# Kernel tuning notes

Hardware: AMD Instinct MI355X
Metric: run time of the kernel (lower is better)

## Reference

```python
import jax, jax.numpy as jnp
import numpy as np

EPS = 1e-5
NUM_HEADS = 16
HEAD_DIM = 64


def layernorm(x, g, b):
    mu = jnp.mean(x, axis=-1, keepdims=True)
    var = jnp.mean(jnp.square(x - mu), axis=-1, keepdims=True)
    return (x - mu) * jax.lax.rsqrt(var + EPS) * g + b


def setup_inputs() -> dict:
    key = jax.random.key(0)
    ks = jax.random.split(key, 10)
    B, S, Q, D = 4, 4096, 256, 1024
    x = jax.random.normal(ks[0], (B, S, D), dtype=jnp.float32)
    queries = jax.random.normal(ks[1], (B, Q, D), dtype=jnp.float32)
    attn_mask = jax.random.randint(ks[2], (B, NUM_HEADS, Q, S), 0, 2) == 1
    key_padding_mask = jax.random.randint(ks[3], (B, S), 0, 2) == 1
    scale = 1.0 / np.sqrt(2.0 * D)  # xavier-ish
    Wq = jax.random.normal(ks[4], (D, D), dtype=jnp.float32) * scale
    Wk = jax.random.normal(ks[5], (D, D), dtype=jnp.float32) * scale
    Wv = jax.random.normal(ks[6], (D, D), dtype=jnp.float32) * scale
    Wo = jax.random.normal(ks[7], (D, D), dtype=jnp.float32) * scale
    ln1_g = jnp.ones((D,), jnp.float32); ln1_b = jnp.zeros((D,), jnp.float32)
    ln2_g = jnp.ones((D,), jnp.float32); ln2_b = jnp.zeros((D,), jnp.float32)
    return {"x": x, "queries": queries, "attn_mask": attn_mask,
            "key_padding_mask": key_padding_mask, "Wq": Wq, "Wk": Wk,
            "Wv": Wv, "Wo": Wo, "ln1_g": ln1_g, "ln1_b": ln1_b,
            "ln2_g": ln2_g, "ln2_b": ln2_b}


def reference(x, queries, attn_mask, key_padding_mask, Wq, Wk, Wv, Wo,
              ln1_g, ln1_b, ln2_g, ln2_b):
    B, S, D = x.shape
    Q = queries.shape[1]
    H, hd = NUM_HEADS, HEAD_DIM

    xn = layernorm(x, ln1_g, ln1_b)
    q = (queries @ Wq.T).reshape(B, Q, H, hd)
    k = (xn @ Wk.T).reshape(B, S, H, hd)
    v = (xn @ Wv.T).reshape(B, S, H, hd)

    # scores: (B, H, Q, S)
    scores = jnp.einsum('bqhd,bshd->bhqs', q, k) / np.sqrt(hd)

    mask = attn_mask | key_padding_mask[:, None, None, :]
    neg_inf = jnp.float32(-jnp.inf)
    masked = jnp.where(mask, neg_inf, scores)
    all_masked = jnp.all(mask, axis=-1, keepdims=True)  # rows fully masked
    safe = jnp.where(all_masked, 0.0, masked)
    attn = jax.nn.softmax(safe, axis=-1)
    attn = jnp.where(all_masked, 0.0, attn)

    out = jnp.einsum('bhqs,bshd->bqhd', attn, v).reshape(B, Q, D)
    out = layernorm(out, ln2_g, ln2_b)
    return out @ Wo.T, attn.mean(axis=1)
```

## Files before the change

kernel.cpp:

```cpp
#include <hip/hip_runtime.h>
#include <math.h>

#define DEV __device__ __forceinline__

typedef float  f4v  __attribute__((ext_vector_type(4)));
typedef __bf16 b8v  __attribute__((ext_vector_type(8)));
typedef short  s8v  __attribute__((ext_vector_type(8)));

DEV short f2b(float f){ __bf16 h = (__bf16)f; return __builtin_bit_cast(short, h); }
DEV float b2f(short s){ __bf16 h = __builtin_bit_cast(__bf16, s); return (float)h; }

DEV void gload16(const void* g, void* l){
  __builtin_amdgcn_global_load_lds((const __attribute__((address_space(1))) void*)g,
                                   (__attribute__((address_space(3))) void*)l, 16, 0, 0);
}

DEV b8v ldsf(const short* p){ return __builtin_bit_cast(b8v, *(const s8v*)p); }

DEV f4v mfma16(b8v a, b8v b, f4v c){ return __builtin_amdgcn_mfma_f32_16x16x32_bf16(a, b, c, 0, 0, 0); }

__global__ void cvt5_kernel(const float* __restrict__ s0, const float* __restrict__ s1,
                            const float* __restrict__ s2, const float* __restrict__ s3,
                            const float* __restrict__ s4,
                            short* __restrict__ d0, short* __restrict__ d1,
                            short* __restrict__ d2, short* __restrict__ d3,
                            short* __restrict__ d4){
  int i = blockIdx.x*256 + threadIdx.x;
  int buf = i >> 18, j = i & 262143;
  const float* s = (buf==0)?s0:(buf==1)?s1:(buf==2)?s2:(buf==3)?s3:s4;
  short*       d = (buf==0)?d0:(buf==1)?d1:(buf==2)?d2:(buf==3)?d3:d4;
  float4 v = ((const float4*)s)[j];
  ((short4*)d)[j] = make_short4(f2b(v.x), f2b(v.y), f2b(v.z), f2b(v.w));
}

__global__ __launch_bounds__(256) void ln_kernel(const float* __restrict__ x, const float* __restrict__ gg,
                                                 const float* __restrict__ bb, short* __restrict__ out){
  int row = blockIdx.x, tid = threadIdx.x;
  const float4 v = ((const float4*)(x + (size_t)row*1024))[tid];
  float s = v.x + v.y + v.z + v.w;
  #pragma unroll
  for (int off=1; off<64; off<<=1) s += __shfl_xor(s, off);
  __shared__ float red[4];
  if ((tid&63)==0) red[tid>>6] = s;
  __syncthreads();
  float mu = (red[0]+red[1]+red[2]+red[3]) * (1.0f/1024.0f);
  float d0=v.x-mu, d1=v.y-mu, d2=v.z-mu, d3=v.w-mu;
  float q = d0*d0 + d1*d1 + d2*d2 + d3*d3;
  #pragma unroll
  for (int off=1; off<64; off<<=1) q += __shfl_xor(q, off);
  __syncthreads();
  if ((tid&63)==0) red[tid>>6] = q;
  __syncthreads();
  float rs = rsqrtf((red[0]+red[1]+red[2]+red[3]) * (1.0f/1024.0f) + 1e-5f);
  float4 g4 = ((const float4*)gg)[tid];
  float4 b4 = ((const float4*)bb)[tid];
  short4 o = make_short4(f2b(d0*rs*g4.x + b4.x), f2b(d1*rs*g4.y + b4.y),
                         f2b(d2*rs*g4.z + b4.z), f2b(d3*rs*g4.w + b4.w));
  ((short4*)(out + (size_t)row*1024))[tid] = o;
}

__global__ __launch_bounds__(256) void ln_reduce_kernel(const short* __restrict__ opart, const float* __restrict__ gg,
                                                        const float* __restrict__ bb, short* __restrict__ out){
  int row = blockIdx.x, tid = threadIdx.x;
  float a0=0.f, a1=0.f, a2=0.f, a3=0.f;
  #pragma unroll
  for (int sc=0; sc<16; ++sc){
    short4 t = ((const short4*)(opart + ((size_t)sc*1024 + row)*1024))[tid];
    a0 += b2f(t.x); a1 += b2f(t.y); a2 += b2f(t.z); a3 += b2f(t.w);
  }
  float s = a0 + a1 + a2 + a3;
  #pragma unroll
  for (int off=1; off<64; off<<=1) s += __shfl_xor(s, off);
  __shared__ float red[4];
  if ((tid&63)==0) red[tid>>6] = s;
  __syncthreads();
  float mu = (red[0]+red[1]+red[2]+red[3]) * (1.0f/1024.0f);
  float d0=a0-mu, d1=a1-mu, d2=a2-mu, d3=a3-mu;
  float q = d0*d0 + d1*d1 + d2*d2 + d3*d3;
  #pragma unroll
  for (int off=1; off<64; off<<=1) q += __shfl_xor(q, off);
  __syncthreads();
  if ((tid&63)==0) red[tid>>6] = q;
  __syncthreads();
  float rs = rsqrtf((red[0]+red[1]+red[2]+red[3]) * (1.0f/1024.0f) + 1e-5f);
  float4 g4 = ((const float4*)gg)[tid];
  float4 b4 = ((const float4*)bb)[tid];
  short4 o = make_short4(f2b(d0*rs*g4.x + b4.x), f2b(d1*rs*g4.y + b4.y),
                         f2b(d2*rs*g4.z + b4.z), f2b(d3*rs*g4.w + b4.w));
  ((short4*)(out + (size_t)row*1024))[tid] = o;
}

template<int OUTF32>
__global__ __launch_bounds__(256) void gemm_small(const short* __restrict__ A, const short* __restrict__ B,
                                                  void* __restrict__ C, int M, int N, int K){
  __shared__ short sA[2][64*64];
  __shared__ short sB[2][64*64];
  int tid=threadIdx.x, lane=tid&63, wv=tid>>6, g=lane>>4, r=lane&15;
  int wr=wv>>1, wc=wv&1;
  int m0=blockIdx.x*64, n0=blockIdx.y*64;
  f4v z = {0.f,0.f,0.f,0.f};
  f4v acc[2][2];
  #pragma unroll
  for (int i=0;i<2;++i){
    #pragma unroll
    for (int j=0;j<2;++j) acc[i][j]=z;
  }
  auto stage = [&](int buf, int kt){
    #pragma unroll
    for (int i=0;i<2;++i){
      int idx = i*256 + tid;
      int row = idx>>3, cbs = (idx&7)^(row&7);
      gload16(A + (size_t)(m0+row)*K + kt*64 + cbs*8, &sA[buf][(i*256+wv*64)*8]);
      gload16(B + (size_t)(n0+row)*K + kt*64 + cbs*8, &sB[buf][(i*256+wv*64)*8]);
    }
  };
  int nkt = K >> 6;
  stage(0, 0);
  __syncthreads();
  for (int kt=0; kt<nkt; ++kt){
    int cur = kt & 1;
    if (kt+1 < nkt) stage(cur^1, kt+1);
    b8v af[2][2], bf[2][2];
    #pragma unroll
    for (int mf=0;mf<2;++mf){
      #pragma unroll
      for (int ks=0;ks<2;++ks){
        int ra = wr*32 + mf*16 + r;
        int rb = wc*32 + mf*16 + r;
        af[mf][ks] = ldsf(&sA[cur][ra*64 + (((ks*4+g)^(ra&7))*8)]);
        bf[mf][ks] = ldsf(&sB[cur][rb*64 + (((ks*4+g)^(rb&7))*8)]);
      }
    }
    #pragma unroll
    for (int mf=0;mf<2;++mf){
      #pragma unroll
      for (int nf=0;nf<2;++nf){
        acc[mf][nf] = mfma16(af[mf][0], bf[nf][0], acc[mf][nf]);
        acc[mf][nf] = mfma16(af[mf][1], bf[nf][1], acc[mf][nf]);
      }
    }
    __syncthreads();
  }
  #pragma unroll
  for (int mf=0;mf<2;++mf){
    #pragma unroll
    for (int nf=0;nf<2;++nf){
      #pragma unroll
      for (int j=0;j<4;++j){
        int m = m0 + wr*32 + mf*16 + g*4 + j;
        int n = n0 + wc*32 + nf*16 + r;
        if (OUTF32) ((float*)C)[(size_t)m*N + n] = acc[mf][nf][j];
        else        ((short*)C)[(size_t)m*N + n] = f2b(acc[mf][nf][j]);
      }
    }
  }
}

__global__ __launch_bounds__(512,2) void gemm_dual_bt(const short* __restrict__ A, const short* __restrict__ B0,
                                                      const short* __restrict__ B1, short* __restrict__ C0,
                                                      short* __restrict__ C1, int M, int N, int K){
  __shared__ short sA[2][256*32];
  __shared__ short sB0[2][128*32];
  __shared__ short sB1[2][128*32];
  int tid=threadIdx.x, lane=tid&63, wv=tid>>6, g=lane>>4, r=lane&15;
  int wr=wv>>1, wc=wv&1;
  int m0=blockIdx.x*256, n0=blockIdx.y*128;
  f4v z = {0.f,0.f,0.f,0.f};
  f4v a0[4][4], a1[4][4];
  #pragma unroll
  for (int i=0;i<4;++i){
    #pragma unroll
    for (int j=0;j<4;++j){ a0[i][j]=z; a1[i][j]=z; }
  }
  auto stage = [&](int buf, int kt){
    #pragma unroll
    for (int i=0;i<2;++i){
      int idx = i*512 + tid;
      int row = idx>>2, sl = idx&3;
      gload16(A + (size_t)(m0+row)*K + kt*32 + sl*8, &sA[buf][(i*512+wv*64)*8]);
    }
    {
      int row = tid>>2, sl = tid&3;
      gload16(B0 + (size_t)(n0+row)*K + kt*32 + sl*8, &sB0[buf][(wv*64)*8]);
      gload16(B1 + (size_t)(n0+row)*K + kt*32 + sl*8, &sB1[buf][(wv*64)*8]);
    }
  };
  int nkt = K >> 5;
  stage(0, 0);
  __syncthreads();
  for (int kt=0; kt<nkt; ++kt){
    int cur = kt & 1;
    if (kt+1 < nkt) stage(cur^1, kt+1);
    b8v af[4], b0f[4], b1f[4];
    #pragma unroll
    for (int mf=0;mf<4;++mf) af[mf] = ldsf(&sA[cur][(wr*64+mf*16+r)*32 + g*8]);
    #pragma unroll
    for (int nf=0;nf<4;++nf){
      b0f[nf] = ldsf(&sB0[cur][(wc*64+nf*16+r)*32 + g*8]);
      b1f[nf] = ldsf(&sB1[cur][(wc*64+nf*16+r)*32 + g*8]);
    }
    #pragma unroll
    for (int mf=0;mf<4;++mf){
      #pragma unroll
      for (int nf=0;nf<4;++nf){
        a0[mf][nf] = mfma16(af[mf], b0f[nf], a0[mf][nf]);
        a1[mf][nf] = mfma16(af[mf], b1f[nf], a1[mf][nf]);
      }
    }
    __syncthreads();
  }
  #pragma unroll
  for (int mf=0;mf<4;++mf){
    #pragma unroll
    for (int nf=0;nf<4;++nf){
      #pragma unroll
      for (int j=0;j<4;++j){
        int m = m0 + wr*64 + mf*16 + g*4 + j;
        int n = n0 + wc*64 + nf*16 + r;
        C0[(size_t)m*N + n] = f2b(a0[mf][nf][j]);
        C1[(size_t)m*N + n] = f2b(a1[mf][nf][j]);
      }
    }
  }
}

__global__ __launch_bounds__(256) void vtrans_kernel(const short* __restrict__ v, short* __restrict__ vt){
  int bid = blockIdx.x;
  int sb = bid & 63, bh = bid >> 6;
  int b = bh >> 4, h = bh & 15;
  int s0 = sb*64;
  __shared__ short t[64][80];
  int tid = threadIdx.x;
  #pragma unroll
  for (int i=0;i<2;++i){
    int idx = tid + i*256;
    int row = idx>>3, sl = idx&7;
    *(s8v*)&t[row][sl*8] = *(const s8v*)(v + (size_t)(b*4096 + s0 + row)*1024 + h*64 + sl*8);
  }
  __syncthreads();
  int hd = tid>>2, part = tid&3;
  s8v o0, o1;
  #pragma unroll
  for (int j=0;j<8;++j){ o0[j] = t[part*16+j][hd]; o1[j] = t[part*16+8+j][hd]; }
  size_t base = (size_t)(bh*64+hd)*4096 + s0 + part*16;
  *(s8v*)(vt + base)     = o0;
  *(s8v*)(vt + base + 8) = o1;
}

__global__ __launch_bounds__(256,2) void lsum_kernel(const short* __restrict__ qp, const short* __restrict__ kb,
                                                     const int* __restrict__ am, const int* __restrict__ kpm,
                                                     unsigned* __restrict__ pm, float* __restrict__ lpart){
  int bid = blockIdx.x;
  int sc = bid & 15, bh = bid >> 4;
  int b = bh >> 4, h = bh & 15;
  int s0 = sc*256;
  __shared__ short sQ[256*64];
  __shared__ short sK[256*64];
  __shared__ unsigned sPM[256*8];
  __shared__ unsigned kw[8];
  int tid=threadIdx.x, lane=tid&63, wv=tid>>6, g=lane>>4, r=lane&15;

  #pragma unroll
  for (int i=0;i<8;++i){
    int idx = i*256 + wv*64 + lane;
    int row = idx>>3, cbs = (idx&7)^(row&7);
    gload16(qp + (size_t)(b*256 + row)*1024 + h*64 + cbs*8, &sQ[(i*256+wv*64)*8]);
  }
  #pragma unroll
  for (int i=0;i<8;++i){
    int idx = i*256 + wv*64 + lane;
    int row = idx>>3, cbs = (idx&7)^(row&7);
    gload16(kb + (size_t)(b*4096 + s0 + row)*1024 + h*64 + cbs*8, &sK[(i*256+wv*64)*8]);
  }
  if (tid < 8){
    unsigned bits = 0;
    const int4* kp = (const int4*)(kpm + (size_t)b*4096 + s0 + tid*32);
    #pragma unroll
    for (int j=0;j<8;++j){
      int4 t = kp[j];
      bits |= (unsigned)(t.x!=0) << (j*4+0);
      bits |= (unsigned)(t.y!=0) << (j*4+1);
      bits |= (unsigned)(t.z!=0) << (j*4+2);
      bits |= (unsigned)(t.w!=0) << (j*4+3);
    }
    kw[tid] = bits;
  }
  unsigned rowbits[8];
  const int4* ap = (const int4*)(am + (size_t)(bh*256 + tid)*4096 + s0);
  #pragma unroll
  for (int w=0;w<8;++w){
    unsigned bits = 0;
    #pragma unroll
    for (int j=0;j<8;++j){
      int4 t = ap[w*8+j];
      bits |= (unsigned)(t.x!=0) << (j*4+0);
      bits |= (unsigned)(t.y!=0) << (j*4+1);
      bits |= (unsigned)(t.z!=0) << (j*4+2);
      bits |= (unsigned)(t.w!=0) << (j*4+3);
    }
    rowbits[w] = bits;
  }
  __syncthreads();
  #pragma unroll
  for (int w=0;w<8;++w){
    unsigned mword = rowbits[w] | kw[w];
    sPM[tid*8+w] = mword;
    pm[(size_t)bid*2048 + tid*8 + w] = mword;
  }
  __syncthreads();

  b8v a[4][2];
  #pragma unroll
  for (int mf=0;mf<4;++mf){
    #pragma unroll
    for (int ks=0;ks<2;++ks){
      int q = wv*64 + mf*16 + r;
      a[mf][ks] = ldsf(&sQ[q*64 + (((ks*4+g)^(q&7))*8)]);
    }
  }
  float lacc[4][4];
  #pragma unroll
  for (int mf=0;mf<4;++mf){
    #pragma unroll
    for (int j=0;j<4;++j) lacc[mf][j] = 0.f;
  }
  f4v z = {0.f,0.f,0.f,0.f};
  #pragma unroll 4
  for (int nf=0;nf<16;++nf){
    int srow = nf*16 + r;
    b8v b0 = ldsf(&sK[srow*64 + ((g^(srow&7))*8)]);
    b8v b1 = ldsf(&sK[srow*64 + (((4+g)^(srow&7))*8)]);
    f4v acc[4];
    #pragma unroll
    for (int mf=0;mf<4;++mf){
      acc[mf] = mfma16(a[mf][0], b0, z);
      acc[mf] = mfma16(a[mf][1], b1, acc[mf]);
    }
    #pragma unroll
    for (int mf=0;mf<4;++mf){
      #pragma unroll
      for (int j=0;j<4;++j){
        int q = wv*64 + mf*16 + g*4 + j;
        unsigned wm = sPM[q*8 + (nf>>1)];
        bool mskd = (wm >> ((nf&1)*16 + r)) & 1u;
        lacc[mf][j] += mskd ? 0.f : __expf(acc[mf][j]*0.125f);
      }
    }
  }
  #pragma unroll
  for (int off=1; off<16; off<<=1){
    #pragma unroll
    for (int mf=0;mf<4;++mf){
      #pragma unroll
      for (int j=0;j<4;++j) lacc[mf][j] += __shfl_xor(lacc[mf][j], off);
    }
  }
  if (r == 0){
    #pragma unroll
    for (int mf=0;mf<4;++mf){
      #pragma unroll
      for (int j=0;j<4;++j){
        int q = wv*64 + mf*16 + g*4 + j;
        lpart[(size_t)bid*256 + q] = lacc[mf][j];
      }
    }
  }
}

__global__ void lcomb_kernel(const float* __restrict__ lpart, float* __restrict__ linv){
  int row = blockIdx.x*256 + threadIdx.x;
  int q = row & 255, bh = row >> 8;
  float l = 0.f;
  #pragma unroll
  for (int sc=0; sc<16; ++sc) l += lpart[(size_t)(bh*16+sc)*256 + q];
  linv[row] = (l > 0.f) ? (1.0f/l) : 0.f;
}

__global__ __launch_bounds__(512,2) void attn_pv_kernel(const short* __restrict__ qp, const short* __restrict__ kb,
                                                        const short* __restrict__ vt, const unsigned* __restrict__ pm,
                                                        const float* __restrict__ linv, short* __restrict__ opart,
                                                        float* __restrict__ out2){
  int bid = blockIdx.x;
  int sc = bid & 15, qt = (bid>>4)&3, b = bid>>6;
  int s0 = sc*256, q0 = qt*64;
  __shared__ short sK[256*64];
  __shared__ short sV[64*256];
  __shared__ short sQ[64*64];
  __shared__ unsigned sPM[64*8];
  int tid=threadIdx.x, lane=tid&63, wv=tid>>6, g=lane>>4, r=lane&15;
  int wq = wv>>2, ws = wv&3;
  f4v z = {0.f,0.f,0.f,0.f};
  float macc[2][4][4];
  #pragma unroll
  for (int mf=0;mf<2;++mf){
    #pragma unroll
    for (int nf=0;nf<4;++nf){
      #pragma unroll
      for (int j=0;j<4;++j) macc[mf][nf][j] = 0.f;
    }
  }

  for (int h=0; h<16; ++h){
    int bh = b*16 + h;
    __syncthreads();
    {
      int row = tid>>3, cbs = (tid&7)^(row&7);
      gload16(qp + (size_t)(b*256 + q0 + row)*1024 + h*64 + cbs*8, &sQ[(wv*64)*8]);
    }
    #pragma unroll
    for (int i=0;i<4;++i){
      int idx = i*512 + tid;
      int row = idx>>3, cbs = (idx&7)^(row&7);
      gload16(kb + (size_t)(b*4096 + s0 + row)*1024 + h*64 + cbs*8, &sK[(i*512+wv*64)*8]);
    }
    #pragma unroll
    for (int i=0;i<4;++i){
      int idx = i*512 + tid;
      int row = idx>>5, sl = idx&31, sls = sl^(row&7);
      gload16(vt + (size_t)(bh*64 + row)*4096 + s0 + sls*8, &sV[(i*512+wv*64)*8]);
    }
    {
      int row = tid>>3, w = tid&7;
      sPM[tid] = pm[(size_t)(bh*16+sc)*2048 + (q0+row)*8 + w];
    }
    __syncthreads();

    b8v aq[2][2];
    #pragma unroll
    for (int mf=0;mf<2;++mf){
      #pragma unroll
      for (int ks=0;ks<2;++ks){
        int qrow = wq*32 + mf*16 + r;
        aq[mf][ks] = ldsf(&sQ[qrow*64 + (((ks*4+g)^(qrow&7))*8)]);
      }
    }
    f4v accs[2][4];
    #pragma unroll
    for (int mf=0;mf<2;++mf){
      #pragma unroll
      for (int nf=0;nf<4;++nf) accs[mf][nf] = z;
    }
    #pragma unroll
    for (int nf=0;nf<4;++nf){
      int srow = ws*64 + nf*16 + r;
      b8v b0 = ldsf(&sK[srow*64 + ((g^(srow&7))*8)]);
      b8v b1 = ldsf(&sK[srow*64 + (((4+g)^(srow&7))*8)]);
      #pragma unroll
      for (int mf=0;mf<2;++mf){
        accs[mf][nf] = mfma16(aq[mf][0], b0, accs[mf][nf]);
        accs[mf][nf] = mfma16(aq[mf][1], b1, accs[mf][nf]);
      }
    }
    __syncthreads();

    #pragma unroll
    for (int mf=0;mf<2;++mf){
      #pragma unroll
      for (int j=0;j<4;++j){
        int ql = wq*32 + mf*16 + g*4 + j;
        float iv = linv[(size_t)bh*256 + q0 + ql];
        #pragma unroll
        for (int nf=0;nf<4;++nf){
          unsigned wm = sPM[ql*8 + ws*2 + (nf>>1)];
          bool mskd = (wm >> ((nf&1)*16 + r)) & 1u;
          float p = mskd ? 0.f : __expf(accs[mf][nf][j]*0.125f) * iv;
          macc[mf][nf][j] += p;
          int sl_ = ws*64 + nf*16 + r;
          sK[ql*256 + (((sl_>>3)^(ql&7))*8) + (sl_&7)] = f2b(p);
        }
      }
    }
    __syncthreads();

    f4v acco[2]; acco[0]=z; acco[1]=z;
    #pragma unroll
    for (int ks=0;ks<8;++ks){
      int vrow = ws*16 + r;
      b8v bv = ldsf(&sV[vrow*256 + (((ks*4+g)^(vrow&7))*8)]);
      #pragma unroll
      for (int mf=0;mf<2;++mf){
        int prow = wq*32 + mf*16 + r;
        b8v ap = ldsf(&sK[prow*256 + (((ks*4+g)^(prow&7))*8)]);
        acco[mf] = mfma16(ap, bv, acco[mf]);
      }
    }
    #pragma unroll
    for (int mf=0;mf<2;++mf){
      #pragma unroll
      for (int j=0;j<4;++j)
        opart[((size_t)sc*1024 + b*256 + q0 + wq*32 + mf*16 + g*4 + j)*1024 + h*64 + ws*16 + r] = f2b(acco[mf][j]);
    }
  }

  #pragma unroll
  for (int mf=0;mf<2;++mf){
    #pragma unroll
    for (int nf=0;nf<4;++nf){
      #pragma unroll
      for (int j=0;j<4;++j){
        int q = q0 + wq*32 + mf*16 + g*4 + j;
        int s = s0 + ws*64 + nf*16 + r;
        out2[(size_t)(b*256 + q)*4096 + s] = macc[mf][nf][j] * 0.0625f;
      }
    }
  }
}

extern "C" void kernel_launch(void* const* d_in, const int* in_sizes, int n_in,
                              void* d_out, int out_size, void* d_ws, size_t ws_size,
                              hipStream_t stream){
  const float* x       = (const float*)d_in[0];
  const float* queries = (const float*)d_in[1];
  const int*   am      = (const int*)d_in[2];
  const int*   kpm     = (const int*)d_in[3];
  const float* Wq      = (const float*)d_in[4];
  const float* Wk      = (const float*)d_in[5];
  const float* Wv      = (const float*)d_in[6];
  const float* Wo      = (const float*)d_in[7];
  const float* ln1g    = (const float*)d_in[8];
  const float* ln1b    = (const float*)d_in[9];
  const float* ln2g    = (const float*)d_in[10];
  const float* ln2b    = (const float*)d_in[11];
  float* out0 = (float*)d_out;
  float* out2 = out0 + (size_t)4*256*1024;
  char* ws = (char*)d_ws;

  size_t off = 0;
  auto alloc = [&](size_t bytes){ void* p = ws + off; off += (bytes + 255) & ~(size_t)255; return p; };
  short*    xn   = (short*)alloc(33554432);
  short*    vt   = xn;
  short*    kb   = (short*)alloc(33554432);
  short*    vb   = (short*)alloc(33554432);
  short*    wqb  = (short*)alloc(2097152);
  short*    wkb  = (short*)alloc(2097152);
  short*    wvb  = (short*)alloc(2097152);
  short*    wob  = (short*)alloc(2097152);
  short*    qbf  = (short*)alloc(2097152);
  short*    qpj  = (short*)alloc(2097152);
  unsigned* pmw  = (unsigned*)alloc(8388608);
  float*    lpart= (float*)alloc(1048576);
  float*    linv = (float*)alloc(65536);
  short*    opart= (short*)alloc(33554432);
  short*    onb  = (short*)alloc(2097152);

  cvt5_kernel<<<5120,256,0,stream>>>(queries, Wq, Wk, Wv, Wo, qbf, wqb, wkb, wvb, wob);
  ln_kernel<<<16384,256,0,stream>>>(x, ln1g, ln1b, xn);
  gemm_dual_bt<<<dim3(64,8),512,0,stream>>>(xn, wkb, wvb, kb, vb, 16384, 1024, 1024);
  gemm_small<0><<<dim3(16,16),256,0,stream>>>(qbf, wqb, qpj, 1024, 1024, 1024);
  vtrans_kernel<<<4096,256,0,stream>>>(vb, vt);
  lsum_kernel<<<1024,256,0,stream>>>(qpj, kb, am, kpm, pmw, lpart);
  lcomb_kernel<<<64,256,0,stream>>>(lpart, linv);
  attn_pv_kernel<<<256,512,0,stream>>>(qpj, kb, vt, pmw, linv, opart, out2);
  ln_reduce_kernel<<<1024,256,0,stream>>>(opart, ln2g, ln2b, onb);
  gemm_small<1><<<dim3(16,16),256,0,stream>>>(onb, wob, out0, 1024, 1024, 1024);
}
```

Measured before the change: 340.1 us.

## Double-buffer attn_pv head loop and build mask bits with coalesced ballots

In attn_pv, the Q, K, V and mask tiles for the next head are prefetched into a second LDS buffer while the current head computes. The QK MFMA is transposed so probabilities are packed and stored to LDS and out2 as vectors, and LDS-only barriers are used between phases. In lsum, the per-thread strided conversion of the mask rows is replaced by lane-coalesced loads combined with __ballot, and mask words are cached in registers for the exp loop. The trade-off is that doubling the LDS buffers (about 148KB) likely allows only one attn_pv block per CU instead of the two requested by the launch bounds.

```diff
diff --git a/kernel.cpp b/kernel.cpp
--- a/kernel.cpp
+++ b/kernel.cpp
@@ -18,6 +18,11 @@
 DEV b8v ldsf(const short* p){ return __builtin_bit_cast(b8v, *(const s8v*)p); }
 
 DEV f4v mfma16(b8v a, b8v b, f4v c){ return __builtin_amdgcn_mfma_f32_16x16x32_bf16(a, b, c, 0, 0, 0); }
+
+DEV void lds_barrier(){
+  asm volatile("s_waitcnt lgkmcnt(0)" ::: "memory");
+  __builtin_amdgcn_s_barrier();
+}
 
 __global__ void cvt5_kernel(const float* __restrict__ s0, const float* __restrict__ s1,
                             const float* __restrict__ s2, const float* __restrict__ s3,
@@ -257,7 +262,6 @@
   __shared__ short sQ[256*64];
   __shared__ short sK[256*64];
   __shared__ unsigned sPM[256*8];
-  __shared__ unsigned kw[8];
   int tid=threadIdx.x, lane=tid&63, wv=tid>>6, g=lane>>4, r=lane&15;
 
   #pragma unroll
@@ -272,40 +276,23 @@
     int row = idx>>3, cbs = (idx&7)^(row&7);
     gload16(kb + (size_t)(b*4096 + s0 + row)*1024 + h*64 + cbs*8, &sK[(i*256+wv*64)*8]);
   }
-  if (tid < 8){
-    unsigned bits = 0;
-    const int4* kp = (const int4*)(kpm + (size_t)b*4096 + s0 + tid*32);
-    #pragma unroll
-    for (int j=0;j<8;++j){
-      int4 t = kp[j];
-      bits |= (unsigned)(t.x!=0) << (j*4+0);
-      bits |= (unsigned)(t.y!=0) << (j*4+1);
-      bits |= (unsigned)(t.z!=0) << (j*4+2);
-      bits |= (unsigned)(t.w!=0) << (j*4+3);
-    }
-    kw[tid] = bits;
-  }
-  unsigned rowbits[8];
-  const int4* ap = (const int4*)(am + (size_t)(bh*256 + tid)*4096 + s0);
-  #pragma unroll
-  for (int w=0;w<8;++w){
-    unsigned bits = 0;
-    #pragma unroll
-    for (int j=0;j<8;++j){
-      int4 t = ap[w*8+j];
-      bits |= (unsigned)(t.x!=0) << (j*4+0);
-      bits |= (unsigned)(t.y!=0) << (j*4+1);
-      bits |= (unsigned)(t.z!=0) << (j*4+2);
-      bits |= (unsigned)(t.w!=0) << (j*4+3);
-    }
-    rowbits[w] = bits;
-  }
-  __syncthreads();
-  #pragma unroll
-  for (int w=0;w<8;++w){
-    unsigned mword = rowbits[w] | kw[w];
-    sPM[tid*8+w] = mword;
-    pm[(size_t)bid*2048 + tid*8 + w] = mword;
+  int4 kp = *(const int4*)(kpm + (size_t)b*4096 + s0 + lane*4);
+  bool k0 = kp.x!=0, k1 = kp.y!=0, k2 = kp.z!=0, k3 = kp.w!=0;
+  #pragma unroll 4
+  for (int i=0;i<64;++i){
+    int row = wv*64 + i;
+    const int4 t = *(const int4*)(am + (size_t)(bh*256 + row)*4096 + s0 + lane*4);
+    unsigned long long m0 = __ballot(k0 || (t.x!=0));
+    unsigned long long m1 = __ballot(k1 || (t.y!=0));
+    unsigned long long m2 = __ballot(k2 || (t.z!=0));
+    unsigned long long m3 = __ballot(k3 || (t.w!=0));
+    if (lane < 8){
+      int jj = lane>>1, hh = lane&1;
+      unsigned long long bj = (jj==0)?m0:((jj==1)?m1:((jj==2)?m2:m3));
+      unsigned w = (unsigned)(bj >> (hh*32));
+      sPM[row*8 + lane] = w;
+      pm[(size_t)bid*2048 + row*8 + lane] = w;
+    }
   }
   __syncthreads();
 
@@ -316,6 +303,16 @@
     for (int ks=0;ks<2;++ks){
       int q = wv*64 + mf*16 + r;
       a[mf][ks] = ldsf(&sQ[q*64 + (((ks*4+g)^(q&7))*8)]);
+    }
+  }
+  unsigned wmr[4][4][2];
+  #pragma unroll
+  for (int mf=0;mf<4;++mf){
+    #pragma unroll
+    for (int jq=0;jq<4;++jq){
+      int q = wv*64 + mf*16 + g*4 + jq;
+      wmr[mf][jq][0] = sPM[q*8 + (r&3)*2 + 0];
+      wmr[mf][jq][1] = sPM[q*8 + (r&3)*2 + 1];
     }
   }
   float lacc[4][4];
@@ -336,13 +333,12 @@
       acc[mf] = mfma16(a[mf][0], b0, z);
       acc[mf] = mfma16(a[mf][1], b1, acc[mf]);
     }
+    int bitp = 4*(nf&7) + (r>>2);
     #pragma unroll
     for (int mf=0;mf<4;++mf){
       #pragma unroll
       for (int j=0;j<4;++j){
-        int q = wv*64 + mf*16 + g*4 + j;
-        unsigned wm = sPM[q*8 + (nf>>1)];
-        bool mskd = (wm >> ((nf&1)*16 + r)) & 1u;
+        bool mskd = (wmr[mf][j][nf>>3] >> bitp) & 1u;
         lacc[mf][j] += mskd ? 0.f : __expf(acc[mf][j]*0.125f);
       }
     }
@@ -383,104 +379,122 @@
   int bid = blockIdx.x;
   int sc = bid & 15, qt = (bid>>4)&3, b = bid>>6;
   int s0 = sc*256, q0 = qt*64;
-  __shared__ short sK[256*64];
-  __shared__ short sV[64*256];
-  __shared__ short sQ[64*64];
-  __shared__ unsigned sPM[64*8];
+  __shared__ short sK[2][256*64];
+  __shared__ short sV[2][64*256];
+  __shared__ short sQ[2][64*64];
+  __shared__ unsigned sPM[2][64*8];
   int tid=threadIdx.x, lane=tid&63, wv=tid>>6, g=lane>>4, r=lane&15;
   int wq = wv>>2, ws = wv&3;
   f4v z = {0.f,0.f,0.f,0.f};
-  float macc[2][4][4];
-  #pragma unroll
-  for (int mf=0;mf<2;++mf){
-    #pragma unroll
-    for (int nf=0;nf<4;++nf){
-      #pragma unroll
-      for (int j=0;j<4;++j) macc[mf][nf][j] = 0.f;
-    }
-  }
-
-  for (int h=0; h<16; ++h){
+  float macc[4][2][4];
+  #pragma unroll
+  for (int sb=0;sb<4;++sb){
+    #pragma unroll
+    for (int qb=0;qb<2;++qb){
+      #pragma unroll
+      for (int j=0;j<4;++j) macc[sb][qb][j] = 0.f;
+    }
+  }
+
+  auto stage = [&](int buf, int h){
     int bh = b*16 + h;
-    __syncthreads();
-    {
-      int row = tid>>3, cbs = (tid&7)^(row&7);
-      gload16(qp + (size_t)(b*256 + q0 + row)*1024 + h*64 + cbs*8, &sQ[(wv*64)*8]);
-    }
+    { int row = tid>>3, cbs = (tid&7)^(row&7);
+      gload16(qp + (size_t)(b*256 + q0 + row)*1024 + h*64 + cbs*8, &sQ[buf][(wv*64)*8]); }
     #pragma unroll
     for (int i=0;i<4;++i){
       int idx = i*512 + tid;
       int row = idx>>3, cbs = (idx&7)^(row&7);
-      gload16(kb + (size_t)(b*4096 + s0 + row)*1024 + h*64 + cbs*8, &sK[(i*512+wv*64)*8]);
+      gload16(kb + (size_t)(b*4096 + s0 + row)*1024 + h*64 + cbs*8, &sK[buf][(i*512+wv*64)*8]);
     }
     #pragma unroll
     for (int i=0;i<4;++i){
       int idx = i*512 + tid;
       int row = idx>>5, sl = idx&31, sls = sl^(row&7);
-      gload16(vt + (size_t)(bh*64 + row)*4096 + s0 + sls*8, &sV[(i*512+wv*64)*8]);
-    }
-    {
-      int row = tid>>3, w = tid&7;
-      sPM[tid] = pm[(size_t)(bh*16+sc)*2048 + (q0+row)*8 + w];
-    }
-    __syncthreads();
-
-    b8v aq[2][2];
-    #pragma unroll
-    for (int mf=0;mf<2;++mf){
+      gload16(vt + (size_t)(bh*64 + row)*4096 + s0 + sls*8, &sV[buf][(i*512+wv*64)*8]);
+    }
+  };
+  auto pmload = [&](int h)->unsigned {
+    return pm[(size_t)((b*16+h)*16+sc)*2048 + (q0 + (tid>>3))*8 + (tid&7)];
+  };
+
+  stage(0, 0);
+  sPM[0][tid] = pmload(0);
+  __syncthreads();
+
+  for (int h=0; h<16; ++h){
+    int cur = h&1;
+    unsigned pmnext = 0;
+    if (h < 15){
+      stage(cur^1, h+1);
+      pmnext = pmload(h+1);
+    }
+    int bh = b*16 + h;
+
+    b8v qf[2][2];
+    #pragma unroll
+    for (int qb=0;qb<2;++qb){
       #pragma unroll
       for (int ks=0;ks<2;++ks){
-        int qrow = wq*32 + mf*16 + r;
-        aq[mf][ks] = ldsf(&sQ[qrow*64 + (((ks*4+g)^(qrow&7))*8)]);
-      }
-    }
-    f4v accs[2][4];
-    #pragma unroll
-    for (int mf=0;mf<2;++mf){
-      #pragma unroll
-      for (int nf=0;nf<4;++nf) accs[mf][nf] = z;
-    }
-    #pragma unroll
-    for (int nf=0;nf<4;++nf){
-      int srow = ws*64 + nf*16 + r;
-      b8v b0 = ldsf(&sK[srow*64 + ((g^(srow&7))*8)]);
-      b8v b1 = ldsf(&sK[srow*64 + (((4+g)^(srow&7))*8)]);
-      #pragma unroll
-      for (int mf=0;mf<2;++mf){
-        accs[mf][nf] = mfma16(aq[mf][0], b0, accs[mf][nf]);
-        accs[mf][nf] = mfma16(aq[mf][1], b1, accs[mf][nf]);
-      }
-    }
-    __syncthreads();
-
-    #pragma unroll
-    for (int mf=0;mf<2;++mf){
-      #pragma unroll
-      for (int j=0;j<4;++j){
-        int ql = wq*32 + mf*16 + g*4 + j;
-        float iv = linv[(size_t)bh*256 + q0 + ql];
+        int qrow = wq*32 + qb*16 + r;
+        qf[qb][ks] = ldsf(&sQ[cur][qrow*64 + (((ks*4+g)^(qrow&7))*8)]);
+      }
+    }
+    f4v accs[4][2];
+    #pragma unroll
+    for (int sb=0;sb<4;++sb){
+      int srow = ws*64 + sb*16 + r;
+      b8v k0 = ldsf(&sK[cur][srow*64 + ((g^(srow&7))*8)]);
+      b8v k1 = ldsf(&sK[cur][srow*64 + (((4+g)^(srow&7))*8)]);
+      #pragma unroll
+      for (int qb=0;qb<2;++qb){
+        accs[sb][qb] = mfma16(k0, qf[qb][0], z);
+        accs[sb][qb] = mfma16(k1, qf[qb][1], accs[sb][qb]);
+      }
+    }
+    lds_barrier();
+
+    float iv[2];
+    iv[0] = linv[(size_t)bh*256 + q0 + wq*32 + r];
+    iv[1] = linv[(size_t)bh*256 + q0 + wq*32 + 16 + r];
+    unsigned wmq[2][4];
+    #pragma unroll
+    for (int qb=0;qb<2;++qb){
+      #pragma unroll
+      for (int j=0;j<4;++j)
+        wmq[qb][j] = sPM[cur][(wq*32+qb*16+r)*8 + j*2 + (ws>>1)];
+    }
+    short* P = &sK[cur][0];
+    #pragma unroll
+    for (int sb=0;sb<4;++sb){
+      int bitp = (ws&1)*16 + sb*4 + g;
+      #pragma unroll
+      for (int qb=0;qb<2;++qb){
+        float pj[4];
         #pragma unroll
-        for (int nf=0;nf<4;++nf){
-          unsigned wm = sPM[ql*8 + ws*2 + (nf>>1)];
-          bool mskd = (wm >> ((nf&1)*16 + r)) & 1u;
-          float p = mskd ? 0.f : __expf(accs[mf][nf][j]*0.125f) * iv;
-          macc[mf][nf][j] += p;
-          int sl_ = ws*64 + nf*16 + r;
-          sK[ql*256 + (((sl_>>3)^(ql&7))*8) + (sl_&7)] = f2b(p);
+        for (int j=0;j<4;++j){
+          bool mskd = (wmq[qb][j] >> bitp) & 1u;
+          pj[j] = mskd ? 0.f : __expf(accs[sb][qb][j]*0.125f) * iv[qb];
+          macc[sb][qb][j] += pj[j];
         }
-      }
-    }
-    __syncthreads();
+        int q = wq*32 + qb*16 + r;
+        unsigned lo = ((unsigned)(unsigned short)f2b(pj[0])) | (((unsigned)(unsigned short)f2b(pj[1]))<<16);
+        unsigned hi = ((unsigned)(unsigned short)f2b(pj[2])) | (((unsigned)(unsigned short)f2b(pj[3]))<<16);
+        int sbase = (ws*64 + sb*16 + g*4) ^ ((q&7)<<3);
+        uint2 pk; pk.x = lo; pk.y = hi;
+        *(uint2*)&P[q*256 + sbase] = pk;
+      }
+    }
+    lds_barrier();
 
     f4v acco[2]; acco[0]=z; acco[1]=z;
     #pragma unroll
     for (int ks=0;ks<8;++ks){
       int vrow = ws*16 + r;
-      b8v bv = ldsf(&sV[vrow*256 + (((ks*4+g)^(vrow&7))*8)]);
+      b8v bv = ldsf(&sV[cur][vrow*256 + (((ks*4+g)^(vrow&7))*8)]);
       #pragma unroll
       for (int mf=0;mf<2;++mf){
         int prow = wq*32 + mf*16 + r;
-        b8v ap = ldsf(&sK[prow*256 + (((ks*4+g)^(prow&7))*8)]);
+        b8v ap = ldsf(&P[prow*256 + ((ks*32+g*8) ^ ((prow&7)<<3))]);
         acco[mf] = mfma16(ap, bv, acco[mf]);
       }
     }
@@ -490,18 +504,18 @@
       for (int j=0;j<4;++j)
         opart[((size_t)sc*1024 + b*256 + q0 + wq*32 + mf*16 + g*4 + j)*1024 + h*64 + ws*16 + r] = f2b(acco[mf][j]);
     }
-  }
-
-  #pragma unroll
-  for (int mf=0;mf<2;++mf){
-    #pragma unroll
-    for (int nf=0;nf<4;++nf){
-      #pragma unroll
-      for (int j=0;j<4;++j){
-        int q = q0 + wq*32 + mf*16 + g*4 + j;
-        int s = s0 + ws*64 + nf*16 + r;
-        out2[(size_t)(b*256 + q)*4096 + s] = macc[mf][nf][j] * 0.0625f;
-      }
+    if (h < 15) sPM[cur^1][tid] = pmnext;
+    __syncthreads();
+  }
+
+  #pragma unroll
+  for (int sb=0;sb<4;++sb){
+    #pragma unroll
+    for (int qb=0;qb<2;++qb){
+      int q = q0 + wq*32 + qb*16 + r;
+      float4 o = make_float4(macc[sb][qb][0]*0.0625f, macc[sb][qb][1]*0.0625f,
+                             macc[sb][qb][2]*0.0625f, macc[sb][qb][3]*0.0625f);
+      *(float4*)&out2[(size_t)(b*256 + q)*4096 + s0 + ws*64 + sb*16 + g*4] = o;
     }
   }
 }
```

Result: no change. 340.6 us (+0.1%).
